# Kernel optimization log

Hardware: AMD Instinct MI355X
Metric: run time of the kernel (lower is better)

## Reference

```python
import jax, jax.numpy as jnp
import numpy as np

SIZE = 8192
M = 1024


def logmatexp(A, B):
    # out[i, j] = logsumexp_k(A[i, k] + B[k, j]), computed stably without
    # materializing the [n, n, m] broadcast tensor:
    # log(exp(A - rowmax_A) @ exp(B - colmax_B)) + rowmax_A + colmax_B
    mA = jnp.max(A, axis=1, keepdims=True)   # [n, 1]
    mB = jnp.max(B, axis=0, keepdims=True)   # [1, m]
    return jnp.log(jnp.exp(A - mA) @ jnp.exp(B - mB)) + mA + mB


def setup_inputs() -> dict:
    key = jax.random.key(0)
    x = jax.random.normal(key, (SIZE, M), dtype=jnp.float32)
    diag = jnp.ones((SIZE,), dtype=jnp.float32)  # nn.Parameter init: ones
    return {"x": x, "diag": diag}


def reference(x, diag):
    # Faithful to forward(): logmatexp(torch.diag(self.diag), x)
    D = jnp.diag(diag)  # dense [SIZE, SIZE], zeros off-diagonal
    return logmatexp(D, x)
```

## Files before the change

kernel.cpp:

```cpp
#include <hip/hip_runtime.h>
#include <hip/hip_bf16.h>
#include <math.h>

#define N_ROWS 8192
#define N_COLS 1024

typedef float f32x4 __attribute__((ext_vector_type(4)));

__global__ __launch_bounds__(1024) void colsum_part(
    const float* __restrict__ x, __hip_bfloat16* __restrict__ ps) {
    const int b    = blockIdx.x;
    const int t    = threadIdx.x;
    const int col0 = (t & 255) * 4;
    const int rg   = t >> 8;
    const int row0 = b * 32 + rg * 8;

    float4 s4 = make_float4(0.f, 0.f, 0.f, 0.f);
#pragma unroll
    for (int k = 0; k < 8; ++k) {
        const float4 v = *reinterpret_cast<const float4*>(
            x + (size_t)(row0 + k) * N_COLS + col0);
        s4.x += __expf(v.x); s4.y += __expf(v.y);
        s4.z += __expf(v.z); s4.w += __expf(v.w);
    }
    __shared__ float red[4][N_COLS];
    *reinterpret_cast<float4*>(&red[rg][col0]) = s4;
    __syncthreads();
    const float s = red[0][t] + red[1][t] + red[2][t] + red[3][t];
    ps[(size_t)b * N_COLS + t] = __float2bfloat16(s);
}

__global__ __launch_bounds__(1024) void merge_finalize(
    const float* __restrict__ x, const float* __restrict__ diag,
    const __hip_bfloat16* __restrict__ ps, float* __restrict__ out) {
    const int cs = blockIdx.x & 7;
    const int rb = blockIdx.x >> 3;
    const int c0 = cs * 128;
    const int t  = threadIdx.x;

    __shared__ float red[16][128];
    __shared__ float S[128];
    {
        const int cg = t >> 6;
        const int cp = t & 63;
        const __hip_bfloat162* ps2 = reinterpret_cast<const __hip_bfloat162*>(ps);
        float s0 = 0.f, s1 = 0.f;
#pragma unroll 8
        for (int k = 0; k < 16; ++k) {
            const __hip_bfloat162 p =
                ps2[(size_t)(cg * 16 + k) * (N_COLS / 2) + cs * 64 + cp];
            s0 += __bfloat162float(p.x);
            s1 += __bfloat162float(p.y);
        }
        red[cg][2 * cp]     = s0;
        red[cg][2 * cp + 1] = s1;
    }
    __syncthreads();
    if (t < 128) {
        float s = 0.f;
#pragma unroll
        for (int g = 0; g < 16; ++g) s += red[g][t];
        S[t] = s;
    }
    __syncthreads();

    const int rr = t >> 5;
    const int cv = t & 31;
    const int col = c0 + 4 * cv;
    const float4 Sj = *reinterpret_cast<const float4*>(&S[4 * cv]);
    const int r0 = rb * 256 + rr;

#pragma unroll
    for (int k = 0; k < 8; ++k) {
        const int row = r0 + k * 32;
        const float E = __expf(diag[row]) - 1.f;
        const size_t off = (size_t)row * N_COLS + col;
        const float4 v = *reinterpret_cast<const float4*>(x + off);
        f32x4 o;
        o.x = __logf(fmaf(E, __expf(v.x), Sj.x));
        o.y = __logf(fmaf(E, __expf(v.y), Sj.y));
        o.z = __logf(fmaf(E, __expf(v.z), Sj.z));
        o.w = __logf(fmaf(E, __expf(v.w), Sj.w));
        __builtin_nontemporal_store(o, reinterpret_cast<f32x4*>(out + off));
    }
}

extern "C" void kernel_launch(void* const* d_in, const int* in_sizes, int n_in,
                              void* d_out, int out_size, void* d_ws, size_t ws_size,
                              hipStream_t stream) {
    const float* x    = (const float*)d_in[0];
    const float* diag = (const float*)d_in[1];
    float* out = (float*)d_out;
    __hip_bfloat16* ps = (__hip_bfloat16*)d_ws;

    colsum_part<<<256, 1024, 0, stream>>>(x, ps);
    merge_finalize<<<256, 1024, 0, stream>>>(x, diag, ps, out);
}
```

Before: 24.70 us.

## Fuse column-sum and finalize into one cooperative kernel with grid barriers

Replaces the two launches with a single cooperative kernel. Each block caches exp(x) for its 32 rows in LDS, writes partial column sums, passes a grid barrier, lets 8 blocks reduce the partials into S, then passes a second barrier before writing the output from the cached exponentials. This removes a kernel launch and the second read of x from global memory. In exchange it adds atomic spin barriers, a memset launch, and a 144KB LDS footprint per block that requires all 256 blocks to be co-resident. It falls back to the old two-kernel path if the cooperative launch fails.

```diff
diff --git a/kernel.cpp b/kernel.cpp
--- a/kernel.cpp
+++ b/kernel.cpp
@@ -4,8 +4,98 @@
 
 #define N_ROWS 8192
 #define N_COLS 1024
+#define NBLK   256
+#define NTHR   1024
 
 typedef float f32x4 __attribute__((ext_vector_type(4)));
+
+__device__ __forceinline__ void grid_barrier(unsigned* ctr, unsigned target) {
+    __syncthreads();
+    if (threadIdx.x == 0) {
+        __threadfence();
+        __hip_atomic_fetch_add(ctr, 1u, __ATOMIC_ACQ_REL, __HIP_MEMORY_SCOPE_AGENT);
+        while (__hip_atomic_load(ctr, __ATOMIC_ACQUIRE, __HIP_MEMORY_SCOPE_AGENT) < target) {
+            __builtin_amdgcn_s_sleep(2);
+        }
+    }
+    __syncthreads();
+}
+
+__global__ __launch_bounds__(NTHR) void fused_manual(
+    const float* __restrict__ x, const float* __restrict__ diag,
+    __hip_bfloat16* __restrict__ ps, float* __restrict__ S,
+    unsigned* __restrict__ ctr, float* __restrict__ out)
+{
+    __shared__ float ex[32][N_COLS];
+    __shared__ float red[4][N_COLS];
+
+    const int t    = threadIdx.x;
+    const int b    = blockIdx.x;
+    const int col0 = (t & 255) * 4;
+    const int rg   = t >> 8;
+    const int r0   = rg * 8;
+    const int row0 = b * 32 + r0;
+
+    float4 s4 = make_float4(0.f, 0.f, 0.f, 0.f);
+#pragma unroll
+    for (int k = 0; k < 8; ++k) {
+        const float4 v = *reinterpret_cast<const float4*>(
+            x + (size_t)(row0 + k) * N_COLS + col0);
+        float4 e;
+        e.x = __expf(v.x); e.y = __expf(v.y);
+        e.z = __expf(v.z); e.w = __expf(v.w);
+        *reinterpret_cast<float4*>(&ex[r0 + k][col0]) = e;
+        s4.x += e.x; s4.y += e.y; s4.z += e.z; s4.w += e.w;
+    }
+    *reinterpret_cast<float4*>(&red[rg][col0]) = s4;
+    __syncthreads();
+    const float sc = red[0][t] + red[1][t] + red[2][t] + red[3][t];
+    ps[(size_t)b * N_COLS + t] = __float2bfloat16(sc);
+
+    grid_barrier(ctr, NBLK);
+
+    if (b < 8) {
+        float (*red2)[128] = reinterpret_cast<float (*)[128]>(&red[0][0]);
+        const int cg = t >> 6;
+        const int cp = t & 63;
+        const __hip_bfloat162* ps2 = reinterpret_cast<const __hip_bfloat162*>(ps);
+        float s0 = 0.f, s1 = 0.f;
+#pragma unroll 8
+        for (int k = 0; k < 16; ++k) {
+            const __hip_bfloat162 p =
+                ps2[(size_t)(cg * 16 + k) * (N_COLS / 2) + b * 64 + cp];
+            s0 += __bfloat162float(p.x);
+            s1 += __bfloat162float(p.y);
+        }
+        red2[cg][2 * cp]     = s0;
+        red2[cg][2 * cp + 1] = s1;
+        __syncthreads();
+        if (t < 128) {
+            float s = 0.f;
+#pragma unroll
+            for (int g = 0; g < 16; ++g) s += red2[g][t];
+            S[b * 128 + t] = s;
+        }
+    }
+
+    grid_barrier(ctr, 2 * NBLK);
+
+    const float4 Sj = *reinterpret_cast<const float4*>(S + col0);
+#pragma unroll
+    for (int k = 0; k < 8; ++k) {
+        const int row = row0 + k;
+        const float E = __expf(diag[row]) - 1.f;
+        const float4 e = *reinterpret_cast<const float4*>(&ex[r0 + k][col0]);
+        f32x4 o;
+        o.x = __logf(fmaf(E, e.x, Sj.x));
+        o.y = __logf(fmaf(E, e.y, Sj.y));
+        o.z = __logf(fmaf(E, e.z, Sj.z));
+        o.w = __logf(fmaf(E, e.w, Sj.w));
+        __builtin_nontemporal_store(
+            o, reinterpret_cast<f32x4*>(out + (size_t)row * N_COLS + col0));
+    }
+}
+
 
 __global__ __launch_bounds__(1024) void colsum_part(
     const float* __restrict__ x, __hip_bfloat16* __restrict__ ps) {
@@ -91,8 +181,19 @@
     const float* x    = (const float*)d_in[0];
     const float* diag = (const float*)d_in[1];
     float* out = (float*)d_out;
-    __hip_bfloat16* ps = (__hip_bfloat16*)d_ws;
 
-    colsum_part<<<256, 1024, 0, stream>>>(x, ps);
-    merge_finalize<<<256, 1024, 0, stream>>>(x, diag, ps, out);
+    unsigned* ctr = (unsigned*)d_ws;
+    __hip_bfloat16* ps = (__hip_bfloat16*)((char*)d_ws + 16);
+    float* S = (float*)((char*)d_ws + 16 + (size_t)NBLK * N_COLS * 2);
+
+    hipMemsetAsync(ctr, 0, sizeof(unsigned), stream);
+
+    void* args[] = { (void*)&x, (void*)&diag, (void*)&ps, (void*)&S,
+                     (void*)&ctr, (void*)&out };
+    hipError_t err = hipLaunchCooperativeKernel((const void*)fused_manual,
+                                                dim3(NBLK), dim3(NTHR), args, 0, stream);
+    if (err != hipSuccess) {
+        colsum_part<<<256, 1024, 0, stream>>>(x, ps);
+        merge_finalize<<<256, 1024, 0, stream>>>(x, diag, ps, out);
+    }
 }
```

Result: slower. 77.36 us (+213.2%).
